# Kernel optimization log

Measured on AMD Instinct MI355X. Metric: run time of the kernel, lower is better.

## Reference

```python
import jax, jax.numpy as jnp
import numpy as np


def setup_inputs() -> dict:
    key = jax.random.key(0)
    k_x, k_q, k_k, k_v = jax.random.split(key, 4)
    B, S, E, D = 4, 2048, 1024, 1024
    scale = 1.0 / np.sqrt(E)
    return {
        "x": jax.random.normal(k_x, (B, S, E), dtype=jnp.float32),
        # nn.Linear weight matrices, shape [out_dim, in_dim]; y = x @ W.T
        "w_q": jax.random.normal(k_q, (D, E), dtype=jnp.float32) * scale,
        "w_k": jax.random.normal(k_k, (D, E), dtype=jnp.float32) * scale,
        "w_v": jax.random.normal(k_v, (D, E), dtype=jnp.float32) * scale,
    }


def reference(x, w_q, w_k, w_v):
    # x: [B, S, E]; w_*: [D, E] (torch nn.Linear convention)
    B, S, E = x.shape
    q = jnp.einsum("bse,de->bsd", x, w_q)  # [B, S, D]
    k = jnp.einsum("bse,de->bsd", x, w_k)
    v = jnp.einsum("bse,de->bsd", x, w_v)
    D = q.shape[-1]
    # raw scores, then causal mask (strictly upper triangle -> -inf), then
    # scale by 1/sqrt(D) inside softmax exactly as the original does.
    scores = jnp.einsum("bsd,btd->bst", q, k)  # [B, S, S]
    causal = jnp.tril(jnp.ones((S, S), dtype=bool))  # True = keep
    scores = jnp.where(causal[None], scores, -jnp.inf)
    attn = jax.nn.softmax(scores / jnp.sqrt(jnp.asarray(D, x.dtype)), axis=-1)
    # dropout p=0.0 -> identity
    return jnp.einsum("bst,btd->bsd", attn, v)  # [B, S, D]
```

## Files before the change

### kernel.cpp

```cpp
#include <hip/hip_runtime.h>
#include <hip/hip_bf16.h>


typedef unsigned short u16;
typedef __attribute__((ext_vector_type(4))) u16   u16x4;
typedef __attribute__((ext_vector_type(8))) u16   u16x8;
typedef __attribute__((ext_vector_type(8))) short short8;
typedef __attribute__((ext_vector_type(4))) float f32x4;
typedef __attribute__((ext_vector_type(4))) int   i32x4;

__device__ inline u16 f2b(float v) {
    __hip_bfloat16 b = __float2bfloat16(v);
    return *reinterpret_cast<u16*>(&b);
}
__device__ inline float b2f(u16 v) {
    unsigned int u = ((unsigned int)v) << 16;
    return *reinterpret_cast<float*>(&u);
}

template <typename T> __device__ inline void store_elem(T* p, float v);
template <> __device__ inline void store_elem<float>(float* p, float v) { *p = v; }
template <> __device__ inline void store_elem<u16>(u16* p, float v)     { *p = f2b(v); }

__device__ inline void gload_lds16(const u16* g, u16* l) {
    __builtin_amdgcn_global_load_lds(
        (const __attribute__((address_space(1))) void*)g,
        (__attribute__((address_space(3))) void*)l, 16, 0, 0);
}

__global__ __launch_bounds__(256) void cast_all_kernel(
    const float* __restrict__ x,  const float* __restrict__ wq,
    const float* __restrict__ wk, const float* __restrict__ wv,
    u16* __restrict__ dst) {
    int q = blockIdx.x * 256 + threadIdx.x;
    const float* src;
    int sidx;
    if (q < 2097152) { src = x; sidx = q * 4; }
    else {
        int qq = q - 2097152;
        int w  = qq >> 18;
        sidx   = (qq & 262143) * 4;
        src    = (w == 0) ? wq : (w == 1) ? wk : wv;
    }
    float4 v = *(const float4*)(src + sidx);
    u16x4 o;
    o.x = f2b(v.x); o.y = f2b(v.y); o.z = f2b(v.z); o.w = f2b(v.w);
    *(u16x4*)(dst + q * 4) = o;
}

__global__ __launch_bounds__(512) void gemm_qk256(
    const u16* __restrict__ xb, const u16* __restrict__ wb,
    u16* __restrict__ qk)
{
    __shared__ __align__(16) u16 lds[2][2][16384];

    const int tid  = threadIdx.x;
    const int lane = tid & 63;
    const int wave = tid >> 6;
    const int quad = lane >> 4;
    const int r16  = lane & 15;
    const int wm   = wave >> 2;
    const int wn   = wave & 3;

    int flat = blockIdx.x;
    int swz  = (flat & 7) * 32 + (flat >> 3);
    int m0   = (swz >> 3) * 256;
    const int n0 = (swz & 7) * 256;
    const u16* __restrict__ Ab = xb;
    const u16* __restrict__ Bb = wb;

    int gA[2][2], gB[2][2], lA[2][2], lB[2][2];
    {
        const int cswz = ((lane & 3) * 8) ^ (((lane >> 5) & 1) << 4);
        const int rsub = lane >> 2;
#pragma unroll
        for (int u = 0; u < 2; ++u)
#pragma unroll
            for (int j = 0; j < 2; ++j) {
                int s   = j * 8 + wave;
                int sh  = s >> 1, cg = s & 1;
                int rgA = (sh & 3) + (sh >> 2) * 8 + u * 4;
                int rgB = sh + u * 8;
                int cl  = cg * 32 + cswz;
                gA[u][j] = (m0 + rgA * 16 + rsub) * 1024 + cl;
                gB[u][j] = (n0 + rgB * 16 + rsub) * 1024 + cl;
                lA[u][j] = (rgA * 2 + cg) * 512 + lane * 8;
                lB[u][j] = (rgB * 2 + cg) * 512 + lane * 8;
            }
    }

#define STAGE_A(BUF, U, KK) do { \
        gload_lds16(Ab + gA[U][0] + (KK), &lds[BUF][0][lA[U][0]]); \
        gload_lds16(Ab + gA[U][1] + (KK), &lds[BUF][0][lA[U][1]]); } while (0)
#define STAGE_B(BUF, U, KK) do { \
        gload_lds16(Bb + gB[U][0] + (KK), &lds[BUF][1][lB[U][0]]); \
        gload_lds16(Bb + gB[U][1] + (KK), &lds[BUF][1][lB[U][1]]); } while (0)

    const int cswr = (quad * 8) ^ ((r16 >> 3) << 4);
    const int rdA0 = wm * 16 * 512 + r16 * 32 + cswr;
    const int rdB0 = wn * 8  * 512 + r16 * 32 + cswr;

    f32x4 acc[8][4] = {};

    STAGE_B(0, 0, 0);  STAGE_B(0, 1, 0);  STAGE_A(0, 0, 0);  STAGE_A(0, 1, 0);
    STAGE_B(1, 0, 64); STAGE_B(1, 1, 64); STAGE_A(1, 0, 64); STAGE_A(1, 1, 64);
    asm volatile("s_waitcnt vmcnt(8)" ::: "memory");
    __builtin_amdgcn_s_barrier();

    for (int t = 0; t < 16; ++t) {
        const int  buf = t & 1;
        const int  kk2 = t * 64 + 128;
        const bool pf  = (t < 14);
        const u16* Al  = lds[buf][0];
        const u16* Bl  = lds[buf][1];
        short8 bfr[4][2], a01[2][2], a23[2][2], a45[2][2], a67[2][2];

#pragma unroll
        for (int nf = 0; nf < 4; ++nf)
#pragma unroll
            for (int ks = 0; ks < 2; ++ks)
                bfr[nf][ks] = *(const short8*)&Bl[rdB0 + (nf * 2 + ks) * 512];
#pragma unroll
        for (int mf = 0; mf < 2; ++mf)
#pragma unroll
            for (int ks = 0; ks < 2; ++ks)
                a01[mf][ks] = *(const short8*)&Al[rdA0 + (mf * 2 + ks) * 512];
        __builtin_amdgcn_s_barrier();
        __builtin_amdgcn_s_setprio(1);
#pragma unroll
        for (int mf = 0; mf < 2; ++mf)
#pragma unroll
            for (int nf = 0; nf < 4; ++nf)
#pragma unroll
                for (int ks = 0; ks < 2; ++ks)
                    acc[mf][nf] = __builtin_amdgcn_mfma_f32_16x16x32_bf16(
                        a01[mf][ks], bfr[nf][ks], acc[mf][nf], 0, 0, 0);
        __builtin_amdgcn_s_setprio(0);
        __builtin_amdgcn_s_barrier();

#pragma unroll
        for (int mf = 0; mf < 2; ++mf)
#pragma unroll
            for (int ks = 0; ks < 2; ++ks)
                a23[mf][ks] = *(const short8*)&Al[rdA0 + ((mf + 2) * 2 + ks) * 512];
        if (pf) STAGE_B(buf, 0, kk2);
        __builtin_amdgcn_s_barrier();
        __builtin_amdgcn_s_setprio(1);
#pragma unroll
        for (int mf = 0; mf < 2; ++mf)
#pragma unroll
            for (int nf = 0; nf < 4; ++nf)
#pragma unroll
                for (int ks = 0; ks < 2; ++ks)
                    acc[mf + 2][nf] = __builtin_amdgcn_mfma_f32_16x16x32_bf16(
                        a23[mf][ks], bfr[nf][ks], acc[mf + 2][nf], 0, 0, 0);
        __builtin_amdgcn_s_setprio(0);
        __builtin_amdgcn_s_barrier();

#pragma unroll
        for (int mf = 0; mf < 2; ++mf)
#pragma unroll
            for (int ks = 0; ks < 2; ++ks) {
                a45[mf][ks] = *(const short8*)&Al[rdA0 + ((mf + 4) * 2 + ks) * 512];
                a67[mf][ks] = *(const short8*)&Al[rdA0 + ((mf + 6) * 2 + ks) * 512];
            }
        if (pf) STAGE_B(buf, 1, kk2);
        __builtin_amdgcn_s_barrier();
        __builtin_amdgcn_s_setprio(1);
#pragma unroll
        for (int mf = 0; mf < 2; ++mf)
#pragma unroll
            for (int nf = 0; nf < 4; ++nf)
#pragma unroll
                for (int ks = 0; ks < 2; ++ks)
                    acc[mf + 4][nf] = __builtin_amdgcn_mfma_f32_16x16x32_bf16(
                        a45[mf][ks], bfr[nf][ks], acc[mf + 4][nf], 0, 0, 0);
        __builtin_amdgcn_s_setprio(0);
        asm volatile("s_waitcnt lgkmcnt(0)" ::: "memory");
        __builtin_amdgcn_s_barrier();

        if (pf) { STAGE_A(buf, 0, kk2); STAGE_A(buf, 1, kk2); }
        __builtin_amdgcn_s_barrier();
        __builtin_amdgcn_s_setprio(1);
#pragma unroll
        for (int mf = 0; mf < 2; ++mf)
#pragma unroll
            for (int nf = 0; nf < 4; ++nf)
#pragma unroll
                for (int ks = 0; ks < 2; ++ks)
                    acc[mf + 6][nf] = __builtin_amdgcn_mfma_f32_16x16x32_bf16(
                        a67[mf][ks], bfr[nf][ks], acc[mf + 6][nf], 0, 0, 0);
        __builtin_amdgcn_s_setprio(0);
        if (pf) asm volatile("s_waitcnt vmcnt(8)" ::: "memory");
        else    asm volatile("s_waitcnt vmcnt(0)" ::: "memory");
        __builtin_amdgcn_s_barrier();
    }
#undef STAGE_A
#undef STAGE_B

#pragma unroll
    for (int mf = 0; mf < 8; ++mf) {
        int m = m0 + wm * 128 + mf * 16 + quad * 4;
#pragma unroll
        for (int nf = 0; nf < 4; ++nf) {
            int n = n0 + wn * 64 + nf * 16 + r16;
#pragma unroll
            for (int r = 0; r < 4; ++r)
                qk[(m + r) * 2048 + n] = f2b(acc[mf][nf][r]);
        }
    }
}

#define MT 128
#define NT 128
#define BKH 32
#define HSZ (MT * BKH)

template <int TRANS, typename OutT>
__device__ __forceinline__ void gemm_core(
    u16* __restrict__ As, u16* __restrict__ Bs,
    const u16* __restrict__ Ab, int lda,
    const u16* __restrict__ Bb, int ldb,
    OutT* __restrict__ Cb, int ldc,
    int m0, int n0, int kbeg, int kend)
{
    const int tid  = threadIdx.x;
    const int lane = tid & 63;
    const int wave = tid >> 6;
    const int quad = lane >> 4;
    const int r16  = lane & 15;
    const int mw   = (wave >> 1) * 64;
    const int nw   = (wave & 1) * 64;

    const int c0 = tid, c1 = tid + 256;
    const int r0 = c0 >> 2, k0 = (c0 & 3) * 8;
    const int r1 = c1 >> 2, k1 = (c1 & 3) * 8;
    const int oa0 = (m0 + r0) * lda + k0;
    const int oa1 = (m0 + r1) * lda + k1;
    const int ob0 = (n0 + r0) * ldb + k0;
    const int ob1 = (n0 + r1) * ldb + k1;

    f32x4 acc[4][4] = {};

    for (int kk = kbeg; kk < kend; kk += 2 * BKH) {
        __syncthreads();
        gload_lds16(Ab + (kk + oa0),        &As[c0 * 8]);
        gload_lds16(Ab + (kk + oa1),        &As[c1 * 8]);
        gload_lds16(Ab + (kk + BKH + oa0),  &As[HSZ + c0 * 8]);
        gload_lds16(Ab + (kk + BKH + oa1),  &As[HSZ + c1 * 8]);
        gload_lds16(Bb + (kk + ob0),        &Bs[c0 * 8]);
        gload_lds16(Bb + (kk + ob1),        &Bs[c1 * 8]);
        gload_lds16(Bb + (kk + BKH + ob0),  &Bs[HSZ + c0 * 8]);
        gload_lds16(Bb + (kk + BKH + ob1),  &Bs[HSZ + c1 * 8]);
        __syncthreads();

#pragma unroll
        for (int h = 0; h < 2; h++) {
            short8 af[4], bf[4];
#pragma unroll
            for (int i = 0; i < 4; i++)
                af[i] = *(const short8*)&As[h * HSZ + (mw + i * 16 + r16) * BKH + quad * 8];
#pragma unroll
            for (int j = 0; j < 4; j++)
                bf[j] = *(const short8*)&Bs[h * HSZ + (nw + j * 16 + r16) * BKH + quad * 8];
#pragma unroll
            for (int i = 0; i < 4; i++)
#pragma unroll
                for (int j = 0; j < 4; j++)
                    acc[i][j] = __builtin_amdgcn_mfma_f32_16x16x32_bf16(af[i], bf[j], acc[i][j], 0, 0, 0);
        }
    }

    if (TRANS == 0) {
#pragma unroll
        for (int i = 0; i < 4; i++)
#pragma unroll
            for (int j = 0; j < 4; j++)
#pragma unroll
                for (int r = 0; r < 4; r++) {
                    int m = m0 + mw + i * 16 + quad * 4 + r;
                    int n = n0 + nw + j * 16 + r16;
                    store_elem(&Cb[(long long)m * ldc + n], acc[i][j][r]);
                }
    } else {
#pragma unroll
        for (int i = 0; i < 4; i++)
#pragma unroll
            for (int j = 0; j < 4; j++) {
                int mbase = m0 + mw + i * 16 + quad * 4;
                int d     = n0 + nw + j * 16 + r16;
                int b     = mbase >> 11;
                int s     = mbase & 2047;
                u16x4 o;
#pragma unroll
                for (int r = 0; r < 4; r++) o[r] = f2b(acc[i][j][r]);
                *(u16x4*)((u16*)Cb + (((b << 10) + d) * 2048 + s)) = o;
            }
    }
}

__global__ __launch_bounds__(256, 4) void gemm_sv(
    const u16* __restrict__ qk, u16* __restrict__ sc,
    const u16* __restrict__ xb, const u16* __restrict__ wb,
    u16* __restrict__ vt) {
    __shared__ __align__(16) u16 As[2 * HSZ];
    __shared__ __align__(16) u16 Bs[2 * HSZ];
    int bid = blockIdx.x;
    if (bid < 544) {
        int z = bid / 136;
        int t = bid - z * 136;
        float ff = sqrtf(8.0f * t + 1.0f);
        int m = (int)((ff - 1.0f) * 0.5f);
        while ((m + 1) * (m + 2) / 2 <= t) m++;
        while (m * (m + 1) / 2 > t) m--;
        int m0 = m * MT;
        int n0 = (t - m * (m + 1) / 2) * NT;
        const u16* Ab = qk + (long long)z * 2048 * 2048;
        const u16* Bb = Ab + 1024;
        u16* Cb = sc + (long long)z * 2048 * 2048;
        gemm_core<0, u16>(As, Bs, Ab, 2048, Bb, 2048, Cb, 2048, m0, n0, 0, 1024);
    } else {
        int vb = bid - 544;
        int bx = vb & 7;
        int m0 = (vb >> 3) * MT;
        gemm_core<1, u16>(As, Bs, xb, 1024, wb + 2048 * 1024, 1024, vt, 2048,
                          m0, bx * 128, 0, 1024);
    }
}

__global__ __launch_bounds__(256, 4) void gemm_pv(
    const u16* __restrict__ P, const u16* __restrict__ vt,
    float* __restrict__ out, float* __restrict__ part)
{
    __shared__ __align__(16) u16 As[2 * HSZ];
    __shared__ __align__(16) u16 Bs[2 * HSZ];
    const int bid = blockIdx.x;
    int m, chunk, n;
    if (bid < 80) {
        int q = bid >> 3; n = bid & 7;
        if (q < 9) { m = 7 + q; chunk = 0; } else { m = 15; chunk = 1; }
    } else {
        int r = bid - 80; int s = 7 - (r >> 4); int t = r & 15;
        n = t & 7;
        if (t < 8) { m = s - 1; chunk = 0; } else { m = s + 7; chunk = 1; }
    }
    const int m0 = m * MT, n0 = n * NT;
    const int kbeg = chunk ? 1024 : 0;
    const int kend = chunk ? (m0 + MT) : min(1024, m0 + MT);
    const int b = blockIdx.z;

    const u16* Ab = P  + (long long)b * 2048 * 2048;
    const u16* Bb = vt + (long long)b * 1024 * 2048;
    float* Cb = (chunk == 0)
        ? out  + (long long)b * 2097152
        : part + (long long)b * 1048576 - 1024LL * 1024;
    gemm_core<0, float>(As, Bs, Ab, 2048, Bb, 2048, Cb, 1024, m0, n0, kbeg, kend);
}

__global__ __launch_bounds__(256) void pv_combine(float* __restrict__ out,
                                                  const float* __restrict__ part) {
    long long idx = ((long long)blockIdx.x * 256 + threadIdx.x) * 8;
    long long bb = idx >> 20;
    long long j  = idx & 1048575;
    float* o = out + bb * 2097152 + 1048576 + j;
    const float* p = part + bb * 1048576 + j;
    float4 o0 = *(float4*)o, o1 = *(float4*)(o + 4);
    float4 p0 = *(const float4*)p, p1 = *(const float4*)(p + 4);
    o0.x += p0.x; o0.y += p0.y; o0.z += p0.z; o0.w += p0.w;
    o1.x += p1.x; o1.y += p1.y; o1.z += p1.z; o1.w += p1.w;
    *(float4*)o = o0; *(float4*)(o + 4) = o1;
}

__device__ __forceinline__ void softmax_row(const u16* __restrict__ sc,
                                            u16* __restrict__ P, int row,
                                            float* __restrict__ red) {
    const int S = 2048;
    int i   = row & (S - 1);
    int n   = i + 1;
    int kendr = (i & ~127) + 128;
    const u16* srow = sc + (long long)row * S;
    u16*       prow = P  + (long long)row * S;

    int j0 = threadIdx.x * 8;
    u16x8 raw = {};
    if (j0 <= i) raw = *(const u16x8*)(srow + j0);
    float v[8];
#pragma unroll
    for (int e = 0; e < 8; e++) v[e] = (j0 + e < n) ? b2f(raw[e]) : -1e30f;

    float lmax = v[0];
#pragma unroll
    for (int e = 1; e < 8; e++) lmax = fmaxf(lmax, v[e]);
    for (int o = 32; o > 0; o >>= 1) lmax = fmaxf(lmax, __shfl_xor(lmax, o, 64));
    int wid = threadIdx.x >> 6;
    if ((threadIdx.x & 63) == 0) red[wid] = lmax;
    __syncthreads();
    float Mx = fmaxf(fmaxf(red[0], red[1]), fmaxf(red[2], red[3]));

    const float C = 0.045112384f;
    float ev[8];
    float lsum = 0.f;
#pragma unroll
    for (int e = 0; e < 8; e++) {
        ev[e] = (j0 + e < n) ? exp2f((v[e] - Mx) * C) : 0.f;
        lsum += ev[e];
    }
    for (int o = 32; o > 0; o >>= 1) lsum += __shfl_xor(lsum, o, 64);
    if ((threadIdx.x & 63) == 0) red[4 + wid] = lsum;
    __syncthreads();
    float inv = 1.0f / (red[4] + red[5] + red[6] + red[7]);

    if (j0 < kendr) {
        u16x8 o8;
#pragma unroll
        for (int e = 0; e < 8; e++) o8[e] = f2b(ev[e] * inv);
        *(u16x8*)(prow + j0) = o8;
    }
}

__global__ __launch_bounds__(256) void softmax_kernel(const u16* __restrict__ sc,
                                                      u16* __restrict__ P) {
    __shared__ float red[8];
    int i = blockIdx.x;
    int z = blockIdx.z;
    softmax_row(sc, P, z * 2048 + (2047 - i), red);
    softmax_row(sc, P, z * 2048 + i, red);
}

extern "C" void kernel_launch(void* const* d_in, const int* in_sizes, int n_in,
                              void* d_out, int out_size, void* d_ws, size_t ws_size,
                              hipStream_t stream) {
    const float* x  = (const float*)d_in[0];
    const float* wq = (const float*)d_in[1];
    const float* wk = (const float*)d_in[2];
    const float* wv = (const float*)d_in[3];
    float* out = (float*)d_out;

    char* ws = (char*)d_ws;
    u16*   xb   = (u16*)(ws);
    u16*   wb   = (u16*)(ws + 16777216LL);
    u16*   qk   = (u16*)(ws + 23068672LL);
    u16*   sc   = (u16*)(ws + 56623104LL);
    u16*   P    = (u16*)(ws + 90177536LL);
    u16*   vt   = (u16*)(ws + 123731968LL);
    float* part = (float*)(ws + 140509184LL);

    cast_all_kernel<<<11264, 256, 0, stream>>>(x, wq, wk, wv, xb);

    gemm_qk256<<<256, 512, 0, stream>>>(xb, wb, qk);

    gemm_sv<<<1056, 256, 0, stream>>>(qk, sc, xb, wb, vt);

    softmax_kernel<<<dim3(1024, 1, 4), 256, 0, stream>>>(sc, P);

    gemm_pv<<<dim3(192, 1, 4), 256, 0, stream>>>(P, vt, out, part);
    pv_combine<<<2048, 256, 0, stream>>>(out, part);
}
```

Before: 247.9 us.

## Use 256x256 tiles for causal QK^T scores and fuse V projection with softmax

Turns the 256-tile bf16 GEMM into a reusable core and runs the causal score GEMM on 256x256 lower-triangular tiles (144 blocks) in place of 128x128 tiles. The V projection is moved into the same launch as the row softmax, so both run concurrently and one kernel launch is dropped. The V tile order is also swizzled. The aim is more data reuse per tile and less launch and tail overhead. The trade-off is wasted work on diagonal tiles at the coarser granularity and a small grid of only 144 blocks for the score GEMM.

```diff
diff --git a/kernel.cpp b/kernel.cpp
--- a/kernel.cpp
+++ b/kernel.cpp
@@ -48,12 +48,13 @@
     *(u16x4*)(dst + q * 4) = o;
 }
 
-__global__ __launch_bounds__(512) void gemm_qk256(
-    const u16* __restrict__ xb, const u16* __restrict__ wb,
-    u16* __restrict__ qk)
-{
-    __shared__ __align__(16) u16 lds[2][2][16384];
-
+__device__ __forceinline__ void gemm256_core(
+    u16* __restrict__ lds,
+    const u16* __restrict__ Ab, int lda,
+    const u16* __restrict__ Bb, int ldb,
+    u16* __restrict__ Cb, int ldc,
+    int m0, int n0)
+{
     const int tid  = threadIdx.x;
     const int lane = tid & 63;
     const int wave = tid >> 6;
@@ -62,13 +63,6 @@
     const int wm   = wave >> 2;
     const int wn   = wave & 3;
 
-    int flat = blockIdx.x;
-    int swz  = (flat & 7) * 32 + (flat >> 3);
-    int m0   = (swz >> 3) * 256;
-    const int n0 = (swz & 7) * 256;
-    const u16* __restrict__ Ab = xb;
-    const u16* __restrict__ Bb = wb;
-
     int gA[2][2], gB[2][2], lA[2][2], lB[2][2];
     {
         const int cswz = ((lane & 3) * 8) ^ (((lane >> 5) & 1) << 4);
@@ -82,19 +76,19 @@
                 int rgA = (sh & 3) + (sh >> 2) * 8 + u * 4;
                 int rgB = sh + u * 8;
                 int cl  = cg * 32 + cswz;
-                gA[u][j] = (m0 + rgA * 16 + rsub) * 1024 + cl;
-                gB[u][j] = (n0 + rgB * 16 + rsub) * 1024 + cl;
+                gA[u][j] = (m0 + rgA * 16 + rsub) * lda + cl;
+                gB[u][j] = (n0 + rgB * 16 + rsub) * ldb + cl;
                 lA[u][j] = (rgA * 2 + cg) * 512 + lane * 8;
                 lB[u][j] = (rgB * 2 + cg) * 512 + lane * 8;
             }
     }
 
 #define STAGE_A(BUF, U, KK) do { \
-        gload_lds16(Ab + gA[U][0] + (KK), &lds[BUF][0][lA[U][0]]); \
-        gload_lds16(Ab + gA[U][1] + (KK), &lds[BUF][0][lA[U][1]]); } while (0)
+        gload_lds16(Ab + gA[U][0] + (KK), lds + (BUF)*32768 + lA[U][0]); \
+        gload_lds16(Ab + gA[U][1] + (KK), lds + (BUF)*32768 + lA[U][1]); } while (0)
 #define STAGE_B(BUF, U, KK) do { \
-        gload_lds16(Bb + gB[U][0] + (KK), &lds[BUF][1][lB[U][0]]); \
-        gload_lds16(Bb + gB[U][1] + (KK), &lds[BUF][1][lB[U][1]]); } while (0)
+        gload_lds16(Bb + gB[U][0] + (KK), lds + (BUF)*32768 + 16384 + lB[U][0]); \
+        gload_lds16(Bb + gB[U][1] + (KK), lds + (BUF)*32768 + 16384 + lB[U][1]); } while (0)
 
     const int cswr = (quad * 8) ^ ((r16 >> 3) << 4);
     const int rdA0 = wm * 16 * 512 + r16 * 32 + cswr;
@@ -111,8 +105,8 @@
         const int  buf = t & 1;
         const int  kk2 = t * 64 + 128;
         const bool pf  = (t < 14);
-        const u16* Al  = lds[buf][0];
-        const u16* Bl  = lds[buf][1];
+        const u16* Al  = lds + buf * 32768;
+        const u16* Bl  = lds + buf * 32768 + 16384;
         short8 bfr[4][2], a01[2][2], a23[2][2], a45[2][2], a67[2][2];
 
 #pragma unroll
@@ -206,9 +200,39 @@
             int n = n0 + wn * 64 + nf * 16 + r16;
 #pragma unroll
             for (int r = 0; r < 4; ++r)
-                qk[(m + r) * 2048 + n] = f2b(acc[mf][nf][r]);
+                Cb[(m + r) * ldc + n] = f2b(acc[mf][nf][r]);
         }
     }
+}
+
+__global__ __launch_bounds__(512) void gemm_qk256(
+    const u16* __restrict__ xb, const u16* __restrict__ wb,
+    u16* __restrict__ qk)
+{
+    __shared__ __align__(16) u16 lds[2 * 2 * 16384];
+    int flat = blockIdx.x;
+    int swz  = (flat & 7) * 32 + (flat >> 3);
+    int m0   = (swz >> 3) * 256;
+    int n0   = (swz & 7) * 256;
+    gemm256_core(lds, xb, 1024, wb, 1024, qk, 2048, m0, n0);
+}
+
+__global__ __launch_bounds__(512) void gemm_sc256(
+    const u16* __restrict__ qk, u16* __restrict__ sc)
+{
+    __shared__ __align__(16) u16 lds[2 * 2 * 16384];
+    int flat = blockIdx.x;
+    int swz  = (flat & 7) * 18 + (flat >> 3);
+    int z    = swz / 36;
+    int t    = swz - z * 36;
+    float ff = sqrtf(8.0f * t + 1.0f);
+    int m = (int)((ff - 1.0f) * 0.5f);
+    while ((m + 1) * (m + 2) / 2 <= t) m++;
+    while (m * (m + 1) / 2 > t) m--;
+    int n = t - m * (m + 1) / 2;
+    const u16* Ab = qk + (long long)z * 2048 * 2048;
+    gemm256_core(lds, Ab, 2048, Ab + 1024, 2048,
+                 sc + (long long)z * 2048 * 2048, 2048, m * 256, n * 256);
 }
 
 #define MT 128
@@ -299,32 +323,73 @@
     }
 }
 
-__global__ __launch_bounds__(256, 4) void gemm_sv(
-    const u16* __restrict__ qk, u16* __restrict__ sc,
+__device__ __forceinline__ void softmax_row(const u16* __restrict__ sc,
+                                            u16* __restrict__ P, int row,
+                                            float* __restrict__ red) {
+    const int S = 2048;
+    int i   = row & (S - 1);
+    int n   = i + 1;
+    int kendr = (i & ~127) + 128;
+    const u16* srow = sc + (long long)row * S;
+    u16*       prow = P  + (long long)row * S;
+
+    int j0 = threadIdx.x * 8;
+    u16x8 raw = {};
+    if (j0 <= i) raw = *(const u16x8*)(srow + j0);
+    float v[8];
+#pragma unroll
+    for (int e = 0; e < 8; e++) v[e] = (j0 + e < n) ? b2f(raw[e]) : -1e30f;
+
+    float lmax = v[0];
+#pragma unroll
+    for (int e = 1; e < 8; e++) lmax = fmaxf(lmax, v[e]);
+    for (int o = 32; o > 0; o >>= 1) lmax = fmaxf(lmax, __shfl_xor(lmax, o, 64));
+    int wid = threadIdx.x >> 6;
+    if ((threadIdx.x & 63) == 0) red[wid] = lmax;
+    __syncthreads();
+    float Mx = fmaxf(fmaxf(red[0], red[1]), fmaxf(red[2], red[3]));
+
+    const float C = 0.045112384f;
+    float ev[8];
+    float lsum = 0.f;
+#pragma unroll
+    for (int e = 0; e < 8; e++) {
+        ev[e] = (j0 + e < n) ? exp2f((v[e] - Mx) * C) : 0.f;
+        lsum += ev[e];
+    }
+    for (int o = 32; o > 0; o >>= 1) lsum += __shfl_xor(lsum, o, 64);
+    if ((threadIdx.x & 63) == 0) red[4 + wid] = lsum;
+    __syncthreads();
+    float inv = 1.0f / (red[4] + red[5] + red[6] + red[7]);
+
+    if (j0 < kendr) {
+        u16x8 o8;
+#pragma unroll
+        for (int e = 0; e < 8; e++) o8[e] = f2b(ev[e] * inv);
+        *(u16x8*)(prow + j0) = o8;
+    }
+}
+
+__global__ __launch_bounds__(256, 4) void v_softmax(
     const u16* __restrict__ xb, const u16* __restrict__ wb,
-    u16* __restrict__ vt) {
+    u16* __restrict__ vt,
+    const u16* __restrict__ sc, u16* __restrict__ P)
+{
     __shared__ __align__(16) u16 As[2 * HSZ];
     __shared__ __align__(16) u16 Bs[2 * HSZ];
     int bid = blockIdx.x;
-    if (bid < 544) {
-        int z = bid / 136;
-        int t = bid - z * 136;
-        float ff = sqrtf(8.0f * t + 1.0f);
-        int m = (int)((ff - 1.0f) * 0.5f);
-        while ((m + 1) * (m + 2) / 2 <= t) m++;
-        while (m * (m + 1) / 2 > t) m--;
-        int m0 = m * MT;
-        int n0 = (t - m * (m + 1) / 2) * NT;
-        const u16* Ab = qk + (long long)z * 2048 * 2048;
-        const u16* Bb = Ab + 1024;
-        u16* Cb = sc + (long long)z * 2048 * 2048;
-        gemm_core<0, u16>(As, Bs, Ab, 2048, Bb, 2048, Cb, 2048, m0, n0, 0, 1024);
+    if (bid < 512) {
+        int vb = (bid & 7) * 64 + (bid >> 3);
+        int m0 = (vb >> 3) * MT;
+        int n0 = (vb & 7) * NT;
+        gemm_core<1, u16>(As, Bs, xb, 1024, wb + 2048 * 1024, 1024, vt, 2048,
+                          m0, n0, 0, 1024);
     } else {
-        int vb = bid - 544;
-        int bx = vb & 7;
-        int m0 = (vb >> 3) * MT;
-        gemm_core<1, u16>(As, Bs, xb, 1024, wb + 2048 * 1024, 1024, vt, 2048,
-                          m0, bx * 128, 0, 1024);
+        float* red = (float*)As;
+        int sid = bid - 512;
+        int z = sid >> 10, i = sid & 1023;
+        softmax_row(sc, P, z * 2048 + (2047 - i), red);
+        softmax_row(sc, P, z * 2048 + i, red);
     }
 }
 
@@ -371,62 +436,6 @@
     *(float4*)o = o0; *(float4*)(o + 4) = o1;
 }
 
-__device__ __forceinline__ void softmax_row(const u16* __restrict__ sc,
-                                            u16* __restrict__ P, int row,
-                                            float* __restrict__ red) {
-    const int S = 2048;
-    int i   = row & (S - 1);
-    int n   = i + 1;
-    int kendr = (i & ~127) + 128;
-    const u16* srow = sc + (long long)row * S;
-    u16*       prow = P  + (long long)row * S;
-
-    int j0 = threadIdx.x * 8;
-    u16x8 raw = {};
-    if (j0 <= i) raw = *(const u16x8*)(srow + j0);
-    float v[8];
-#pragma unroll
-    for (int e = 0; e < 8; e++) v[e] = (j0 + e < n) ? b2f(raw[e]) : -1e30f;
-
-    float lmax = v[0];
-#pragma unroll
-    for (int e = 1; e < 8; e++) lmax = fmaxf(lmax, v[e]);
-    for (int o = 32; o > 0; o >>= 1) lmax = fmaxf(lmax, __shfl_xor(lmax, o, 64));
-    int wid = threadIdx.x >> 6;
-    if ((threadIdx.x & 63) == 0) red[wid] = lmax;
-    __syncthreads();
-    float Mx = fmaxf(fmaxf(red[0], red[1]), fmaxf(red[2], red[3]));
-
-    const float C = 0.045112384f;
-    float ev[8];
-    float lsum = 0.f;
-#pragma unroll
-    for (int e = 0; e < 8; e++) {
-        ev[e] = (j0 + e < n) ? exp2f((v[e] - Mx) * C) : 0.f;
-        lsum += ev[e];
-    }
-    for (int o = 32; o > 0; o >>= 1) lsum += __shfl_xor(lsum, o, 64);
-    if ((threadIdx.x & 63) == 0) red[4 + wid] = lsum;
-    __syncthreads();
-    float inv = 1.0f / (red[4] + red[5] + red[6] + red[7]);
-
-    if (j0 < kendr) {
-        u16x8 o8;
-#pragma unroll
-        for (int e = 0; e < 8; e++) o8[e] = f2b(ev[e] * inv);
-        *(u16x8*)(prow + j0) = o8;
-    }
-}
-
-__global__ __launch_bounds__(256) void softmax_kernel(const u16* __restrict__ sc,
-                                                      u16* __restrict__ P) {
-    __shared__ float red[8];
-    int i = blockIdx.x;
-    int z = blockIdx.z;
-    softmax_row(sc, P, z * 2048 + (2047 - i), red);
-    softmax_row(sc, P, z * 2048 + i, red);
-}
-
 extern "C" void kernel_launch(void* const* d_in, const int* in_sizes, int n_in,
                               void* d_out, int out_size, void* d_ws, size_t ws_size,
                               hipStream_t stream) {
@@ -449,9 +458,9 @@
 
     gemm_qk256<<<256, 512, 0, stream>>>(xb, wb, qk);
 
-    gemm_sv<<<1056, 256, 0, stream>>>(qk, sc, xb, wb, vt);
-
-    softmax_kernel<<<dim3(1024, 1, 4), 256, 0, stream>>>(sc, P);
+    gemm_sc256<<<144, 512, 0, stream>>>(qk, sc);
+
+    v_softmax<<<4608, 256, 0, stream>>>(xb, wb, vt, sc, P);
 
     gemm_pv<<<dim3(192, 1, 4), 256, 0, stream>>>(P, vt, out, part);
     pv_combine<<<2048, 256, 0, stream>>>(out, part);
```

Result: faster. 235.5 us (-5.0%).
